# Kernel optimization log

Measured on AMD Instinct MI355X. Metric: run time of the kernel, lower is better.

## Reference

```python
import jax, jax.numpy as jnp
import numpy as np

# dims: H heads, D=word_size (d_model), E=embed_dim per head, N=seq_len=n, K=linformer k
H, D, E, N, K = 16, 1024, 64, 4096, 256


def setup_inputs() -> dict:
    key = jax.random.key(0)
    ks = jax.random.split(key, 9)
    s = 0.02  # init scale for weights
    return {
        "x":  jax.random.normal(ks[0], (N, D), jnp.float32),
        # per-head QKV linears: torch Linear weight is (out=E, in=D), bias (E,)
        "Wq": jax.random.normal(ks[1], (H, E, D), jnp.float32) * s,
        "bq": jnp.zeros((H, E), jnp.float32),
        "Wk": jax.random.normal(ks[2], (H, E, D), jnp.float32) * s,
        "bk": jnp.zeros((H, E), jnp.float32),
        "Wv": jax.random.normal(ks[3], (H, E, D), jnp.float32) * s,
        "bv": jnp.zeros((H, E), jnp.float32),
        # per-head E/F sequence projections: Linear(n=N, k=K) -> weight (K, N), bias (K,)
        "Ew": jax.random.normal(ks[4], (H, K, N), jnp.float32) * s,
        "Eb": jnp.zeros((H, K), jnp.float32),
        "Fw": jax.random.normal(ks[5], (H, K, N), jnp.float32) * s,
        "Fb": jnp.zeros((H, K), jnp.float32),
        # output projection: Linear(H*E, E, bias=False) -> weight (E, H*E)
        "Wo": jax.random.normal(ks[6], (E, H * E), jnp.float32) * s,
    }


def reference(x, Wq, bq, Wk, bk, Wv, bv, Ew, Eb, Fw, Fb, Wo):
    # per-head Q/K/V projections, batched over heads: (H, N, E)
    q = jnp.einsum('nd,hed->hne', x, Wq) + bq[:, None, :]
    k = jnp.einsum('nd,hed->hne', x, Wk) + bk[:, None, :]
    v = jnp.einsum('nd,hed->hne', x, Wv) + bv[:, None, :]
    # low-rank sequence-length projection of K and V: (H, K, E)
    kp = jnp.einsum('hjn,hne->hje', Ew, k) + Eb[:, :, None]
    vp = jnp.einsum('hjn,hne->hje', Fw, v) + Fb[:, :, None]
    # scaled dot-product attention against projected keys: (H, N, K)
    score = jnp.einsum('hne,hje->hnj', q, kp) / jnp.sqrt(jnp.float32(E))
    attn = jax.nn.softmax(score, axis=-1)
    z = jnp.einsum('hnj,hje->hne', attn, vp)  # (H, N, E)
    # concat heads along feature dim (matches torch.cat(dim=1)): (N, H*E)
    zs = jnp.transpose(z, (1, 0, 2)).reshape(N, H * E)
    # final projection Linear(H*E, E, bias=False)
    return zs @ Wo.T  # (N, E)
```

## Files before the change

### kernel.cpp

```cpp
#include <hip/hip_runtime.h>
#include <hip/hip_bf16.h>

typedef __attribute__((ext_vector_type(4))) float f32x4;
typedef __attribute__((ext_vector_type(8))) short s16x8;
typedef __attribute__((ext_vector_type(4))) short s16x4;
typedef unsigned short u16;


__device__ __forceinline__ f32x4 mfma16(s16x8 a, s16x8 b, f32x4 c) {
    return __builtin_amdgcn_mfma_f32_16x16x32_bf16(a, b, c, 0, 0, 0);
}

__device__ __forceinline__ u16 bf(float f) {
    union { float f; unsigned u; } x; x.f = f;
    return (u16)((x.u + 0x7fffu + ((x.u >> 16) & 1u)) >> 16);
}
__device__ __forceinline__ unsigned pkbf(float a, float b) {
    union { float f; unsigned u; } x, y; x.f = a; y.f = b;
    unsigned ra = x.u + 0x7fffu + ((x.u >> 16) & 1u);
    unsigned rb = y.u + 0x7fffu + ((y.u >> 16) & 1u);
    return (ra >> 16) | (rb & 0xffff0000u);
}
__device__ __forceinline__ s16x8 cvt8(f32x4 lo, f32x4 hi) {
    union { s16x8 v; unsigned u[4]; } r;
    r.u[0] = pkbf(lo.x, lo.y);
    r.u[1] = pkbf(lo.z, lo.w);
    r.u[2] = pkbf(hi.x, hi.y);
    r.u[3] = pkbf(hi.z, hi.w);
    return r.v;
}

__device__ __forceinline__ void gl_lds16(const u16* g, u16* l) {
    __builtin_amdgcn_global_load_lds(
        (const __attribute__((address_space(1))) unsigned*)g,
        (__attribute__((address_space(3))) unsigned*)l, 16, 0, 0);
}


__global__ __launch_bounds__(256) void cvt_kernel(const float* __restrict__ src,
                                                  u16* __restrict__ dst, int n4) {
    int i = blockIdx.x * 256 + threadIdx.x;
    if (i < n4) {
        f32x4 v = ((const f32x4*)src)[i];
        union { s16x4 v; unsigned u[2]; } r;
        r.u[0] = pkbf(v.x, v.y);
        r.u[1] = pkbf(v.z, v.w);
        ((s16x4*)dst)[i] = r.v;
    }
}


__global__ __launch_bounds__(256, 3) void qkv_kernel(
        const u16* __restrict__ xb, const u16* __restrict__ wb,
        const float* __restrict__ bq, const float* __restrict__ bk,
        const float* __restrict__ bv,
        u16* __restrict__ qo, u16* __restrict__ kTo, u16* __restrict__ vTo) {
    __shared__ u16 As[128 * 32];
    __shared__ u16 Bs[128 * 32];
    int bx   = blockIdx.x % 24;
    int by   = blockIdx.x / 24;
    int tid  = threadIdx.x;
    int lane = tid & 63, w = tid >> 6;
    int l15  = lane & 15, quad = lane >> 4;
    int wr   = w >> 1, wc = w & 1;

    const u16* Ag = xb + (size_t)(by * 128 + (tid >> 2)) * 1024 + (tid & 3) * 8;
    const u16* Bg = wb + (size_t)(bx * 128 + (tid >> 2)) * 1024 + (tid & 3) * 8;
    u16* Al = As + tid * 8;
    u16* Bl = Bs + tid * 8;

    const u16* abase = As + (wr * 64 + l15) * 32 + quad * 8;
    const u16* bbase = Bs + (wc * 64 + l15) * 32 + quad * 8;

    f32x4 acc[4][4] = {};
    for (int k0 = 0; k0 < 1024; k0 += 32) {
        gl_lds16(Ag + k0, Al);
        gl_lds16(Ag + 64 * 1024 + k0, Al + 64 * 32);
        gl_lds16(Bg + k0, Bl);
        gl_lds16(Bg + 64 * 1024 + k0, Bl + 64 * 32);
        __syncthreads();
        s16x8 a[4], b[4];
#pragma unroll
        for (int mi = 0; mi < 4; mi++) a[mi] = *(const s16x8*)(abase + mi * 16 * 32);
#pragma unroll
        for (int nj = 0; nj < 4; nj++) b[nj] = *(const s16x8*)(bbase + nj * 16 * 32);
#pragma unroll
        for (int mi = 0; mi < 4; mi++)
#pragma unroll
            for (int nj = 0; nj < 4; nj++) acc[mi][nj] = mfma16(a[mi], b[nj], acc[mi][nj]);
        __syncthreads();
    }

    int fblk = (bx * 128 + wc * 64) >> 6;
    int mat  = fblk >> 4, h = fblk & 15;
    const float* bias = (mat == 0) ? bq : (mat == 1 ? bk : bv);
#pragma unroll
    for (int nj = 0; nj < 4; nj++) {
        int e = nj * 16 + l15;
        float bb = bias[h * 64 + e];
#pragma unroll
        for (int mi = 0; mi < 4; mi++) {
            int n0 = by * 128 + wr * 64 + mi * 16 + quad * 4;
            f32x4 c = acc[mi][nj];
            if (mat == 0) {
                u16* p = qo + ((size_t)h * 4096 + n0) * 64 + e;
#pragma unroll
                for (int r = 0; r < 4; r++) p[(size_t)r * 64] = bf(c[r] + bb);
            } else {
                u16* p = (mat == 1 ? kTo : vTo) + ((size_t)h * 64 + e) * 4096 + n0;
                union { s16x4 v; u16 s[4]; } pk;
#pragma unroll
                for (int r = 0; r < 4; r++) pk.s[r] = bf(c[r] + bb);
                *(s16x4*)p = pk.v;
            }
        }
    }
}


__global__ __launch_bounds__(256, 4) void kpvp_kernel(
        const float* __restrict__ Ew, const float* __restrict__ Fw,
        const u16* __restrict__ kT, const u16* __restrict__ vT,
        float* __restrict__ accs) {
    __shared__ u16 As[128 * 40];
    __shared__ u16 Bs[64 * 32];
    int b    = blockIdx.x;
    int ks   = b & 15, jt = (b >> 4) & 1, h = (b >> 5) & 15, p = b >> 9;
    int tid  = threadIdx.x;
    int lane = tid & 63, w = tid >> 6;
    int l15  = lane & 15, quad = lane >> 4;
    int wm   = w & 1, wn = w >> 1;

    const float* Ag = (p ? Fw : Ew)
        + (size_t)(h * 256 + jt * 128 + (tid >> 3)) * 4096 + ks * 256 + (tid & 7) * 4;
    const u16* Bg = (p ? vT : kT)
        + ((size_t)h * 64 + (tid >> 2)) * 4096 + ks * 256 + (tid & 3) * 8;
    u16* Aw = As + (tid >> 3) * 40 + (tid & 7) * 4;
    u16* Bl = Bs + tid * 8;

    const u16* abase = As + (wm * 64 + l15) * 40 + quad * 8;
    const u16* bbase = Bs + (wn * 32 + l15) * 32 + quad * 8;

    f32x4 acc[4][2] = {};
    for (int s = 0; s < 8; s++) {
        int kk = s * 32;
        gl_lds16(Bg + kk, Bl);
#pragma unroll
        for (int pr = 0; pr < 4; pr++) {
            f32x4 v = *(const f32x4*)(Ag + (size_t)pr * 32 * 4096 + kk);
            union { s16x4 q; unsigned u[2]; } rr;
            rr.u[0] = pkbf(v.x, v.y);
            rr.u[1] = pkbf(v.z, v.w);
            *(s16x4*)(Aw + pr * 32 * 40) = rr.q;
        }
        __syncthreads();
        s16x8 a[4], bb2[2];
#pragma unroll
        for (int mt = 0; mt < 4; mt++) a[mt] = *(const s16x8*)(abase + mt * 16 * 40);
#pragma unroll
        for (int nt = 0; nt < 2; nt++) bb2[nt] = *(const s16x8*)(bbase + nt * 16 * 32);
#pragma unroll
        for (int mt = 0; mt < 4; mt++)
#pragma unroll
            for (int nt = 0; nt < 2; nt++)
                acc[mt][nt] = mfma16(a[mt], bb2[nt], acc[mt][nt]);
        __syncthreads();
    }

    size_t base = (size_t)ks * 524288
        + ((size_t)(p * 16 + h) * 256 + jt * 128 + wm * 64 + quad * 4) * 64
        + wn * 32 + l15;
#pragma unroll
    for (int mt = 0; mt < 4; mt++)
#pragma unroll
        for (int nt = 0; nt < 2; nt++)
#pragma unroll
            for (int r = 0; r < 4; r++)
                accs[base + (size_t)(mt * 16 + r) * 64 + nt * 16] = acc[mt][nt][r];
}


__global__ __launch_bounds__(256) void packkv_kernel(
        const float* __restrict__ accs, const float* __restrict__ Eb,
        const float* __restrict__ Fb, u16* __restrict__ kp, u16* __restrict__ vpT) {
    int idx = blockIdx.x * 256 + threadIdx.x;
    float v = 0.f;
#pragma unroll
    for (int s = 0; s < 16; s++) v += accs[idx + (size_t)s * 524288];
    int p = idx >> 18, h = (idx >> 14) & 15, j = (idx >> 6) & 255, e = idx & 63;
    if (p == 0) {
        v += Eb[h * 256 + j];
        kp[((size_t)(h * 256 + j)) * 64 + e] = bf(v * 0.125f);
    } else {
        v += Fb[h * 256 + j];
        vpT[((size_t)(h * 64 + e)) * 256 + j] = bf(v);
    }
}


__global__ __launch_bounds__(256) void attn_kernel(
        const u16* __restrict__ q, const u16* __restrict__ kp,
        const u16* __restrict__ vpT, u16* __restrict__ zs) {
    __shared__ u16 ps[4][16][256];
    int bm   = blockIdx.x & 63, h = blockIdx.x >> 6;
    int lane = threadIdx.x & 63, w = threadIdx.x >> 6;
    int l15  = lane & 15, quad = lane >> 4;
    int nbase = bm * 64 + w * 16;

    f32x4 s[16] = {};
    const u16* qp  = q  + ((size_t)h * 4096 + nbase + l15) * 64 + quad * 8;
    const u16* kpp = kp + ((size_t)h * 256 + l15) * 64 + quad * 8;
#pragma unroll
    for (int e0 = 0; e0 < 64; e0 += 32) {
        s16x8 a = *(const s16x8*)(qp + e0);
#pragma unroll
        for (int jt = 0; jt < 16; jt++) {
            s16x8 b = *(const s16x8*)(kpp + jt * 16 * 64 + e0);
            s[jt] = mfma16(a, b, s[jt]);
        }
    }

    float lsum[4];
#pragma unroll
    for (int r = 0; r < 4; r++) {
        float m = s[0][r];
#pragma unroll
        for (int jt = 1; jt < 16; jt++) m = fmaxf(m, s[jt][r]);
        m = fmaxf(m, __shfl_xor(m, 1));
        m = fmaxf(m, __shfl_xor(m, 2));
        m = fmaxf(m, __shfl_xor(m, 4));
        m = fmaxf(m, __shfl_xor(m, 8));
        float l = 0.f;
#pragma unroll
        for (int jt = 0; jt < 16; jt++) {
            float pv = __expf(s[jt][r] - m);
            s[jt][r] = pv;
            l += pv;
        }
        l += __shfl_xor(l, 1);
        l += __shfl_xor(l, 2);
        l += __shfl_xor(l, 4);
        l += __shfl_xor(l, 8);
        lsum[r] = l;
    }

#pragma unroll
    for (int jt = 0; jt < 16; jt++)
#pragma unroll
        for (int r = 0; r < 4; r++)
            ps[w][quad * 4 + r][jt * 16 + l15] = bf(s[jt][r]);
    __syncthreads();

    f32x4 z[4] = {};
    const u16* vp = vpT + ((size_t)h * 64 + l15) * 256 + quad * 8;
#pragma unroll
    for (int kj = 0; kj < 8; kj++) {
        s16x8 a = *(const s16x8*)&ps[w][l15][kj * 32 + quad * 8];
#pragma unroll
        for (int et = 0; et < 4; et++) {
            s16x8 b = *(const s16x8*)(vp + et * 16 * 256 + kj * 32);
            z[et] = mfma16(a, b, z[et]);
        }
    }
#pragma unroll
    for (int et = 0; et < 4; et++) {
        int e = et * 16 + l15;
        u16* o = zs + ((size_t)(nbase + quad * 4)) * 1024 + h * 64 + e;
#pragma unroll
        for (int r = 0; r < 4; r++) o[(size_t)r * 1024] = bf(z[et][r] / lsum[r]);
    }
}


__global__ __launch_bounds__(256) void out_kernel(
        const u16* __restrict__ zs, const u16* __restrict__ wob,
        float* __restrict__ out) {
    int ks   = blockIdx.x & 3;
    int bm   = blockIdx.x >> 2;
    int lane = threadIdx.x & 63, w = threadIdx.x >> 6;
    int l15  = lane & 15, quad = lane >> 4;
    int row0 = bm * 128 + w * 32;

    const u16* A = zs  + (size_t)(row0 + l15) * 1024 + ks * 256 + quad * 8;
    const u16* B = wob + (size_t)l15 * 1024 + ks * 256 + quad * 8;

    f32x4 acc[2][4] = {};
    for (int k = 0; k < 256; k += 32) {
        s16x8 a0 = *(const s16x8*)(A + k);
        s16x8 a1 = *(const s16x8*)(A + 16 * 1024 + k);
#pragma unroll
        for (int nt = 0; nt < 4; nt++) {
            s16x8 bv = *(const s16x8*)(B + (size_t)nt * 16 * 1024 + k);
            acc[0][nt] = mfma16(a0, bv, acc[0][nt]);
            acc[1][nt] = mfma16(a1, bv, acc[1][nt]);
        }
    }
#pragma unroll
    for (int mt = 0; mt < 2; mt++)
#pragma unroll
        for (int nt = 0; nt < 4; nt++) {
            int e = nt * 16 + l15;
            int n0 = row0 + mt * 16 + quad * 4;
            float* o = out + (size_t)n0 * 64 + e;
#pragma unroll
            for (int r = 0; r < 4; r++) atomicAdd(o + (size_t)r * 64, acc[mt][nt][r]);
        }
}


extern "C" void kernel_launch(void* const* d_in, const int* in_sizes, int n_in,
                              void* d_out, int out_size, void* d_ws, size_t ws_size,
                              hipStream_t stream) {
    const float* x  = (const float*)d_in[0];
    const float* Wq = (const float*)d_in[1];
    const float* bq = (const float*)d_in[2];
    const float* Wk = (const float*)d_in[3];
    const float* bk = (const float*)d_in[4];
    const float* Wv = (const float*)d_in[5];
    const float* bv = (const float*)d_in[6];
    const float* Ew = (const float*)d_in[7];
    const float* Eb = (const float*)d_in[8];
    const float* Fw = (const float*)d_in[9];
    const float* Fb = (const float*)d_in[10];
    const float* Wo = (const float*)d_in[11];

    char* ws = (char*)d_ws;
    u16*   qb   = (u16*)(ws + 0);
    u16*   kT   = (u16*)(ws + 8388608);
    u16*   vT   = (u16*)(ws + 16777216);
    u16*   zsb  = (u16*)(ws + 25165824);
    float* accs = (float*)(ws + 33554432);
    u16*   kp   = (u16*)(ws + 67108864);
    u16*   vpT  = (u16*)(ws + 67633152);
    u16*   xb   = (u16*)(ws + 68157440);
    u16*   wb   = (u16*)(ws + 76546048);
    u16*   wob  = (u16*)(ws + 82837504);

    hipMemsetAsync(d_out, 0, (size_t)4096 * 64 * sizeof(float), stream);

    cvt_kernel<<<4096, 256, 0, stream>>>(x,  xb, 1048576);
    cvt_kernel<<<1024, 256, 0, stream>>>(Wq, wb,           262144);
    cvt_kernel<<<1024, 256, 0, stream>>>(Wk, wb + 1048576, 262144);
    cvt_kernel<<<1024, 256, 0, stream>>>(Wv, wb + 2097152, 262144);
    cvt_kernel<<<64,   256, 0, stream>>>(Wo, wob, 16384);

    qkv_kernel<<<768, 256, 0, stream>>>(xb, wb, bq, bk, bv, qb, kT, vT);
    kpvp_kernel<<<1024, 256, 0, stream>>>(Ew, Fw, kT, vT, accs);
    packkv_kernel<<<2048, 256, 0, stream>>>(accs, Eb, Fb, kp, vpT);
    attn_kernel<<<1024, 256, 0, stream>>>(qb, kp, vpT, zsb);
    out_kernel<<<128, 256, 0, stream>>>(zsb, wob, (float*)d_out);
}
```

Measured before the change: 311.3 us.

## Merge conversion kernels, widen kpvp tiles, replace output atomics with slice reduction

Folds the five fp32-to-bf16 conversion launches into one kernel and drops the output memset. The kpvp kernel now covers all 256 projected rows per block, halving the grid so each block reuses its K/V tile across twice as many rows, at lower occupancy. The output projection writes per-split partial slices into the workspace, and a new small kernel sums them, replacing float atomics. This adds one launch and extra workspace traffic in exchange for fewer launches and no atomic contention.

```diff
diff --git a/kernel.cpp b/kernel.cpp
--- a/kernel.cpp
+++ b/kernel.cpp
@@ -21,14 +21,6 @@
     unsigned rb = y.u + 0x7fffu + ((y.u >> 16) & 1u);
     return (ra >> 16) | (rb & 0xffff0000u);
 }
-__device__ __forceinline__ s16x8 cvt8(f32x4 lo, f32x4 hi) {
-    union { s16x8 v; unsigned u[4]; } r;
-    r.u[0] = pkbf(lo.x, lo.y);
-    r.u[1] = pkbf(lo.z, lo.w);
-    r.u[2] = pkbf(hi.x, hi.y);
-    r.u[3] = pkbf(hi.z, hi.w);
-    return r.v;
-}
 
 __device__ __forceinline__ void gl_lds16(const u16* g, u16* l) {
     __builtin_amdgcn_global_load_lds(
@@ -37,16 +29,24 @@
 }
 
 
-__global__ __launch_bounds__(256) void cvt_kernel(const float* __restrict__ src,
-                                                  u16* __restrict__ dst, int n4) {
+__global__ __launch_bounds__(256) void cvt_all_kernel(
+        const float* __restrict__ x,  const float* __restrict__ Wq,
+        const float* __restrict__ Wk, const float* __restrict__ Wv,
+        const float* __restrict__ Wo,
+        u16* __restrict__ xb, u16* __restrict__ wb, u16* __restrict__ wob) {
     int i = blockIdx.x * 256 + threadIdx.x;
-    if (i < n4) {
-        f32x4 v = ((const f32x4*)src)[i];
-        union { s16x4 v; unsigned u[2]; } r;
-        r.u[0] = pkbf(v.x, v.y);
-        r.u[1] = pkbf(v.z, v.w);
-        ((s16x4*)dst)[i] = r.v;
-    }
+    const float* src; u16* dst; int off;
+    if (i < 1048576)      { src = x;  dst = xb;            off = i; }
+    else if (i < 1310720) { src = Wq; dst = wb;            off = i - 1048576; }
+    else if (i < 1572864) { src = Wk; dst = wb + 1048576;  off = i - 1310720; }
+    else if (i < 1835008) { src = Wv; dst = wb + 2097152;  off = i - 1572864; }
+    else if (i < 1851392) { src = Wo; dst = wob;           off = i - 1835008; }
+    else return;
+    f32x4 v = ((const f32x4*)src)[off];
+    union { s16x4 v; unsigned u[2]; } r;
+    r.u[0] = pkbf(v.x, v.y);
+    r.u[1] = pkbf(v.z, v.w);
+    ((s16x4*)dst)[off] = r.v;
 }
 
 
@@ -118,35 +118,34 @@
 }
 
 
-__global__ __launch_bounds__(256, 4) void kpvp_kernel(
+__global__ __launch_bounds__(256, 2) void kpvp_kernel(
         const float* __restrict__ Ew, const float* __restrict__ Fw,
         const u16* __restrict__ kT, const u16* __restrict__ vT,
         float* __restrict__ accs) {
-    __shared__ u16 As[128 * 40];
+    __shared__ u16 As[256 * 40];
     __shared__ u16 Bs[64 * 32];
     int b    = blockIdx.x;
-    int ks   = b & 15, jt = (b >> 4) & 1, h = (b >> 5) & 15, p = b >> 9;
+    int ks   = b & 15, h = (b >> 4) & 15, p = b >> 8;
     int tid  = threadIdx.x;
     int lane = tid & 63, w = tid >> 6;
     int l15  = lane & 15, quad = lane >> 4;
-    int wm   = w & 1, wn = w >> 1;
 
     const float* Ag = (p ? Fw : Ew)
-        + (size_t)(h * 256 + jt * 128 + (tid >> 3)) * 4096 + ks * 256 + (tid & 7) * 4;
+        + (size_t)(h * 256 + (tid >> 3)) * 4096 + ks * 256 + (tid & 7) * 4;
     const u16* Bg = (p ? vT : kT)
         + ((size_t)h * 64 + (tid >> 2)) * 4096 + ks * 256 + (tid & 3) * 8;
     u16* Aw = As + (tid >> 3) * 40 + (tid & 7) * 4;
     u16* Bl = Bs + tid * 8;
 
-    const u16* abase = As + (wm * 64 + l15) * 40 + quad * 8;
-    const u16* bbase = Bs + (wn * 32 + l15) * 32 + quad * 8;
-
-    f32x4 acc[4][2] = {};
+    const u16* abase = As + (w * 64 + l15) * 40 + quad * 8;
+    const u16* bbase = Bs + l15 * 32 + quad * 8;
+
+    f32x4 acc[4][4] = {};
     for (int s = 0; s < 8; s++) {
         int kk = s * 32;
         gl_lds16(Bg + kk, Bl);
 #pragma unroll
-        for (int pr = 0; pr < 4; pr++) {
+        for (int pr = 0; pr < 8; pr++) {
             f32x4 v = *(const f32x4*)(Ag + (size_t)pr * 32 * 4096 + kk);
             union { s16x4 q; unsigned u[2]; } rr;
             rr.u[0] = pkbf(v.x, v.y);
@@ -154,26 +153,25 @@
             *(s16x4*)(Aw + pr * 32 * 40) = rr.q;
         }
         __syncthreads();
-        s16x8 a[4], bb2[2];
+        s16x8 a[4], bb2[4];
 #pragma unroll
         for (int mt = 0; mt < 4; mt++) a[mt] = *(const s16x8*)(abase + mt * 16 * 40);
 #pragma unroll
-        for (int nt = 0; nt < 2; nt++) bb2[nt] = *(const s16x8*)(bbase + nt * 16 * 32);
+        for (int nt = 0; nt < 4; nt++) bb2[nt] = *(const s16x8*)(bbase + nt * 16 * 32);
 #pragma unroll
         for (int mt = 0; mt < 4; mt++)
 #pragma unroll
-            for (int nt = 0; nt < 2; nt++)
+            for (int nt = 0; nt < 4; nt++)
                 acc[mt][nt] = mfma16(a[mt], bb2[nt], acc[mt][nt]);
         __syncthreads();
     }
 
     size_t base = (size_t)ks * 524288
-        + ((size_t)(p * 16 + h) * 256 + jt * 128 + wm * 64 + quad * 4) * 64
-        + wn * 32 + l15;
+        + ((size_t)(p * 16 + h) * 256 + w * 64 + quad * 4) * 64 + l15;
 #pragma unroll
     for (int mt = 0; mt < 4; mt++)
 #pragma unroll
-        for (int nt = 0; nt < 2; nt++)
+        for (int nt = 0; nt < 4; nt++)
 #pragma unroll
             for (int r = 0; r < 4; r++)
                 accs[base + (size_t)(mt * 16 + r) * 64 + nt * 16] = acc[mt][nt][r];
@@ -274,7 +272,7 @@
 
 __global__ __launch_bounds__(256) void out_kernel(
         const u16* __restrict__ zs, const u16* __restrict__ wob,
-        float* __restrict__ out) {
+        float* __restrict__ oslice) {
     int ks   = blockIdx.x & 3;
     int bm   = blockIdx.x >> 2;
     int lane = threadIdx.x & 63, w = threadIdx.x >> 6;
@@ -295,16 +293,23 @@
             acc[1][nt] = mfma16(a1, bv, acc[1][nt]);
         }
     }
+    float* os = oslice + (size_t)ks * 262144;
 #pragma unroll
     for (int mt = 0; mt < 2; mt++)
 #pragma unroll
         for (int nt = 0; nt < 4; nt++) {
             int e = nt * 16 + l15;
             int n0 = row0 + mt * 16 + quad * 4;
-            float* o = out + (size_t)n0 * 64 + e;
-#pragma unroll
-            for (int r = 0; r < 4; r++) atomicAdd(o + (size_t)r * 64, acc[mt][nt][r]);
-        }
+            float* o = os + (size_t)n0 * 64 + e;
+#pragma unroll
+            for (int r = 0; r < 4; r++) o[(size_t)r * 64] = acc[mt][nt][r];
+        }
+}
+
+__global__ __launch_bounds__(256) void outred_kernel(
+        const float* __restrict__ oslice, float* __restrict__ out) {
+    int i = blockIdx.x * 256 + threadIdx.x;
+    out[i] = oslice[i] + oslice[i + 262144] + oslice[i + 524288] + oslice[i + 786432];
 }
 
 
@@ -336,17 +341,11 @@
     u16*   wb   = (u16*)(ws + 76546048);
     u16*   wob  = (u16*)(ws + 82837504);
 
-    hipMemsetAsync(d_out, 0, (size_t)4096 * 64 * sizeof(float), stream);
-
-    cvt_kernel<<<4096, 256, 0, stream>>>(x,  xb, 1048576);
-    cvt_kernel<<<1024, 256, 0, stream>>>(Wq, wb,           262144);
-    cvt_kernel<<<1024, 256, 0, stream>>>(Wk, wb + 1048576, 262144);
-    cvt_kernel<<<1024, 256, 0, stream>>>(Wv, wb + 2097152, 262144);
-    cvt_kernel<<<64,   256, 0, stream>>>(Wo, wob, 16384);
-
+    cvt_all_kernel<<<7232, 256, 0, stream>>>(x, Wq, Wk, Wv, Wo, xb, wb, wob);
     qkv_kernel<<<768, 256, 0, stream>>>(xb, wb, bq, bk, bv, qb, kT, vT);
-    kpvp_kernel<<<1024, 256, 0, stream>>>(Ew, Fw, kT, vT, accs);
+    kpvp_kernel<<<512, 256, 0, stream>>>(Ew, Fw, kT, vT, accs);
     packkv_kernel<<<2048, 256, 0, stream>>>(accs, Eb, Fb, kp, vpT);
     attn_kernel<<<1024, 256, 0, stream>>>(qb, kp, vpT, zsb);
-    out_kernel<<<128, 256, 0, stream>>>(zsb, wob, (float*)d_out);
-}
+    out_kernel<<<128, 256, 0, stream>>>(zsb, wob, (float*)accs);
+    outred_kernel<<<1024, 256, 0, stream>>>((const float*)accs, (float*)d_out);
+}
```

Measured after the change: 299.4 us. -3.8%, faster.
